# Optimization experiments

Hardware: AMD Instinct MI355X
Metric: run time of the kernel (lower is better)

## Reference

```python
import jax, jax.numpy as jnp
import numpy as np

HEAD_DIM = 64
NUM_HEADS = 32
ROPE_BASE = 10000.0


def _rope_interleaved(x):
    # x: [B, T, H, D]; interleaved RoPE on query, seqlen_offset = 0
    B, T, H, D = x.shape
    inv_freq = 1.0 / (ROPE_BASE ** (jnp.arange(0, D, 2, dtype=jnp.float32) / D))  # [D/2]
    t = jnp.arange(T, dtype=jnp.float32)
    freqs = t[:, None] * inv_freq[None, :]          # [T, D/2]
    cos = jnp.cos(freqs)[None, :, None, :]          # [1, T, 1, D/2]
    sin = jnp.sin(freqs)[None, :, None, :]
    x1 = x[..., 0::2]
    x2 = x[..., 1::2]
    o1 = x1 * cos - x2 * sin
    o2 = x1 * sin + x2 * cos
    out = jnp.stack([o1, o2], axis=-1).reshape(x.shape)  # re-interleave
    return out


def setup_inputs() -> dict:
    key = jax.random.key(0)
    k1, k2, k3, k4, k5 = jax.random.split(key, 5)
    B, T, Dm = 2, 2048, 2048
    H, Dh = NUM_HEADS, HEAD_DIM
    scale = 0.02
    return {
        "hidden_states": jax.random.normal(k1, (B, T, Dm), jnp.float32),
        "shared_k": jax.random.normal(k2, (B, T, H, Dh), jnp.float32),
        "shared_v": jax.random.normal(k3, (B, T, H, Dh), jnp.float32),
        "Wq": jax.random.normal(k4, (Dm, Dm), jnp.float32) * scale,
        "Wo": jax.random.normal(k5, (Dm, Dm), jnp.float32) * scale,
    }


def reference(hidden_states, shared_k, shared_v, Wq, Wo):
    B, T, Dm = hidden_states.shape
    H, Dh = NUM_HEADS, HEAD_DIM
    # q projection (nn.Linear: x @ W.T)
    q = (hidden_states @ Wq.T).reshape(B, T, H, Dh)
    # rotary on q only (seqlen_offset = shared_k_len - q_len = 0)
    q = _rope_interleaved(q)
    # parallel causal attention over shared KV cache (window_size=None)
    scale = 1.0 / jnp.sqrt(jnp.asarray(Dh, jnp.float32))
    scores = jnp.einsum('bqhd,bkhd->bhqk', q, shared_k) * scale
    causal = jnp.tril(jnp.ones((T, T), dtype=bool))
    scores = jnp.where(causal[None, None], scores, -jnp.inf)
    p = jax.nn.softmax(scores, axis=-1)
    o = jnp.einsum('bhqk,bkhd->bqhd', p, shared_v)
    o = o.reshape(B, T, Dm)
    return o @ Wo.T
```

## Files before the change

kernel.cpp:

```cpp
#include <hip/hip_runtime.h>
#include <stdint.h>

typedef short short8 __attribute__((ext_vector_type(8)));
typedef float f32x4 __attribute__((ext_vector_type(4)));

#define QSCALE 0.1803368801111137f

__device__ __forceinline__ float bf2f(unsigned short u) {
    union { unsigned int i; float f; } x; x.i = ((unsigned int)u) << 16; return x.f;
}
__device__ __forceinline__ unsigned short f2bf(float f) {
    union { float f; unsigned int i; } x; x.f = f;
    unsigned int i = x.i;
    unsigned int r = i + 0x7FFFu + ((i >> 16) & 1u);
    return (unsigned short)(r >> 16);
}

#define GLDS16(g, l) \
    __builtin_amdgcn_global_load_lds((const __attribute__((address_space(1))) void*)(g), \
                                     (__attribute__((address_space(3))) void*)(l), 16, 0, 0)

__global__ void cvt_f32_bf16(const float* __restrict__ in, unsigned short* __restrict__ out, int n4) {
    int i = blockIdx.x * 256 + threadIdx.x;
    if (i >= n4) return;
    float4 v = ((const float4*)in)[i];
    ushort4 o;
    o.x = f2bf(v.x); o.y = f2bf(v.y); o.z = f2bf(v.z); o.w = f2bf(v.w);
    ((ushort4*)out)[i] = o;
}

__global__ __launch_bounds__(256) void transpose_v(const float* __restrict__ V, unsigned short* __restrict__ Vt) {
    __shared__ float s[64 * 65];
    int t0 = blockIdx.x * 64;
    int bh = blockIdx.y;
    int b = bh >> 5, h = bh & 31;
    int tid = threadIdx.x;
#pragma unroll
    for (int it = 0; it < 4; ++it) {
        int c = tid + it * 256;
        int t = c >> 4;
        int d0 = (c & 15) * 4;
        float4 v = *(const float4*)(V + (size_t)(((b * 2048 + t0 + t) * 32 + h)) * 64 + d0);
        s[t * 65 + d0 + 0] = v.x; s[t * 65 + d0 + 1] = v.y;
        s[t * 65 + d0 + 2] = v.z; s[t * 65 + d0 + 3] = v.w;
    }
    __syncthreads();
#pragma unroll
    for (int it = 0; it < 2; ++it) {
        int c = tid + it * 256;
        int d = c >> 3;
        int tt = (c & 7) * 8;
        short8 pk;
#pragma unroll
        for (int j = 0; j < 8; ++j) pk[j] = (short)f2bf(s[(tt + j) * 65 + d]);
        *(short8*)(Vt + (size_t)(bh * 64 + d) * 2048 + t0 + tt) = pk;
    }
}

__global__ void rope_table(float* __restrict__ ct, float* __restrict__ st) {
    int i = blockIdx.x * 256 + threadIdx.x;
    int t = i >> 5, fi = i & 31;
    float inv = powf(10000.0f, -(2.0f * (float)fi) / 64.0f);
    float ang = (float)t * inv;
    ct[i] = cosf(ang);
    st[i] = sinf(ang);
}

__global__ void rope_apply(unsigned short* __restrict__ Q, const float* __restrict__ ct, const float* __restrict__ st) {
    int p = blockIdx.x * 256 + threadIdx.x;
    int row = p >> 10;
    int j = p & 1023;
    int t = row & 2047;
    int h = j >> 5, fi = j & 31;
    int col = h * 64 + fi * 2;
    unsigned int* addr = (unsigned int*)(Q + (size_t)row * 2048 + col);
    unsigned int v = *addr;
    float x1 = bf2f((unsigned short)(v & 0xffffu));
    float x2 = bf2f((unsigned short)(v >> 16));
    float c = ct[t * 32 + fi], s = st[t * 32 + fi];
    float o1 = (x1 * c - x2 * s) * QSCALE;
    float o2 = (x1 * s + x2 * c) * QSCALE;
    *addr = (unsigned int)f2bf(o1) | ((unsigned int)f2bf(o2) << 16);
}

template <bool BF16_OUT>
__global__ __launch_bounds__(256) void gemm_bt(
    const unsigned short* __restrict__ A,
    const unsigned short* __restrict__ B,
    void* __restrict__ Cout,
    int M, int N, int K)
{
    __shared__ __align__(16) unsigned short lA[128 * 32];
    __shared__ __align__(16) unsigned short lB[128 * 32];
    int tid = threadIdx.x;
    int lane = tid & 63;
    int wave = tid >> 6;
    int wm = (wave >> 1) * 64, wn = (wave & 1) * 64;
    int m16 = lane & 15, q = lane >> 4;
    int rowBase = blockIdx.x * 128, colBase = blockIdx.y * 128;

    f32x4 acc[4][4] = {};

    int sRow = wave * 16 + (lane >> 2);
    int sCol = (lane & 3) * 8;
    const unsigned short* gA0 = A + (size_t)(rowBase + sRow) * K + sCol;
    const unsigned short* gA1 = gA0 + (size_t)64 * K;
    const unsigned short* gB0 = B + (size_t)(colBase + sRow) * K + sCol;
    const unsigned short* gB1 = gB0 + (size_t)64 * K;
    unsigned short* lA0 = &lA[(wave * 16) * 32];
    unsigned short* lA1 = &lA[(64 + wave * 16) * 32];
    unsigned short* lB0 = &lB[(wave * 16) * 32];
    unsigned short* lB1 = &lB[(64 + wave * 16) * 32];

    for (int k0 = 0; k0 < K; k0 += 32) {
        __syncthreads();
        GLDS16(gA0 + k0, lA0);
        GLDS16(gA1 + k0, lA1);
        GLDS16(gB0 + k0, lB0);
        GLDS16(gB1 + k0, lB1);
        __syncthreads();
        short8 af[4], bfr[4];
#pragma unroll
        for (int i = 0; i < 4; ++i) {
            af[i]  = *(const short8*)&lA[(wm + i * 16 + m16) * 32 + q * 8];
            bfr[i] = *(const short8*)&lB[(wn + i * 16 + m16) * 32 + q * 8];
        }
#pragma unroll
        for (int i = 0; i < 4; ++i)
#pragma unroll
            for (int jn = 0; jn < 4; ++jn)
                acc[i][jn] = __builtin_amdgcn_mfma_f32_16x16x32_bf16(af[i], bfr[jn], acc[i][jn], 0, 0, 0);
    }
#pragma unroll
    for (int i = 0; i < 4; ++i)
#pragma unroll
        for (int jn = 0; jn < 4; ++jn)
#pragma unroll
            for (int r = 0; r < 4; ++r) {
                int row = rowBase + wm + i * 16 + q * 4 + r;
                int col = colBase + wn + jn * 16 + m16;
                float v = acc[i][jn][r];
                if (BF16_OUT) ((unsigned short*)Cout)[(size_t)row * N + col] = f2bf(v);
                else          ((float*)Cout)[(size_t)row * N + col] = v;
            }
}

__global__ __launch_bounds__(256) void attn(
    const unsigned short* __restrict__ Q,
    const unsigned short* __restrict__ Kb,
    const unsigned short* __restrict__ Vt,
    unsigned short* __restrict__ O)
{
    const int SL = 80;
    __shared__ __align__(16) unsigned short sK[64 * SL];
    __shared__ __align__(16) unsigned short sV[64 * SL];
    __shared__ __align__(16) unsigned short sP[4][16 * SL];
    int tid = threadIdx.x, lane = tid & 63, w = tid >> 6;
    int m16 = lane & 15, q = lane >> 4;
    int flat = blockIdx.x;
    int qt = 31 - (flat >> 6);
    int bh = flat & 63;
    int b = bh >> 5, h = bh & 31;
    int qBase = qt * 64;

    size_t rowQ = (size_t)(b * 2048 + qBase + w * 16 + m16) * 2048 + h * 64 + q * 8;
    short8 aq0 = *(const short8*)(Q + rowQ);
    short8 aq1 = *(const short8*)(Q + rowQ + 32);

    float lrun[4] = {0.f, 0.f, 0.f, 0.f};
    f32x4 accO[4];
#pragma unroll
    for (int nt = 0; nt < 4; ++nt) { f32x4 z = {0.f, 0.f, 0.f, 0.f}; accO[nt] = z; }

    int cK = tid >> 3;
    int c8 = tid & 7;
    const unsigned short* kbase = Kb + (size_t)(b * 2048) * 2048 + h * 64;
    const unsigned short* vbase = Vt + (size_t)((b * 32 + h) * 64) * 2048;

    for (int kt = 0; kt <= qt; ++kt) {
        int kBase = kt * 64;
        __syncthreads();
#pragma unroll
        for (int it = 0; it < 2; ++it) {
            int row = cK + it * 32;
            *(float4*)&sK[row * SL + c8 * 8] =
                *(const float4*)(kbase + (size_t)(kBase + row) * 2048 + c8 * 8);
            *(float4*)&sV[row * SL + c8 * 8] =
                *(const float4*)(vbase + (size_t)row * 2048 + kBase + c8 * 8);
        }
        __syncthreads();

        f32x4 accS[4];
#pragma unroll
        for (int nt = 0; nt < 4; ++nt) {
            f32x4 z = {0.f, 0.f, 0.f, 0.f};
            short8 bk0 = *(const short8*)&sK[(nt * 16 + m16) * SL + q * 8];
            short8 bk1 = *(const short8*)&sK[(nt * 16 + m16) * SL + 32 + q * 8];
            z = __builtin_amdgcn_mfma_f32_16x16x32_bf16(aq0, bk0, z, 0, 0, 0);
            z = __builtin_amdgcn_mfma_f32_16x16x32_bf16(aq1, bk1, z, 0, 0, 0);
            accS[nt] = z;
        }

        bool diag = (kt == qt);
#pragma unroll
        for (int nt = 0; nt < 4; ++nt)
#pragma unroll
            for (int r = 0; r < 4; ++r) {
                float s = accS[nt][r];
                if (diag) {
                    int key = nt * 16 + m16;
                    int qi = w * 16 + q * 4 + r;
                    if (key > qi) s = -__builtin_inff();
                }
                float p = __builtin_amdgcn_exp2f(s);
                lrun[r] += p;
                sP[w][(q * 4 + r) * SL + nt * 16 + m16] = f2bf(p);
            }

        short8 ap0 = *(const short8*)&sP[w][m16 * SL + q * 8];
        short8 ap1 = *(const short8*)&sP[w][m16 * SL + 32 + q * 8];
#pragma unroll
        for (int nt = 0; nt < 4; ++nt) {
            short8 bv0 = *(const short8*)&sV[(nt * 16 + m16) * SL + q * 8];
            short8 bv1 = *(const short8*)&sV[(nt * 16 + m16) * SL + 32 + q * 8];
            accO[nt] = __builtin_amdgcn_mfma_f32_16x16x32_bf16(ap0, bv0, accO[nt], 0, 0, 0);
            accO[nt] = __builtin_amdgcn_mfma_f32_16x16x32_bf16(ap1, bv1, accO[nt], 0, 0, 0);
        }
    }

#pragma unroll
    for (int r = 0; r < 4; ++r) {
        float l = lrun[r];
        l += __shfl_xor(l, 1);
        l += __shfl_xor(l, 2);
        l += __shfl_xor(l, 4);
        l += __shfl_xor(l, 8);
        lrun[r] = 1.0f / l;
    }
#pragma unroll
    for (int nt = 0; nt < 4; ++nt)
#pragma unroll
        for (int r = 0; r < 4; ++r) {
            float v = accO[nt][r] * lrun[r];
            O[(size_t)(b * 2048 + qBase + w * 16 + q * 4 + r) * 2048 + h * 64 + nt * 16 + m16] = f2bf(v);
        }
}

extern "C" void kernel_launch(void* const* d_in, const int* in_sizes, int n_in,
                              void* d_out, int out_size, void* d_ws, size_t ws_size,
                              hipStream_t stream) {
    const float* hs = (const float*)d_in[0];
    const float* sk = (const float*)d_in[1];
    const float* sv = (const float*)d_in[2];
    const float* wq = (const float*)d_in[3];
    const float* wo = (const float*)d_in[4];
    float* out = (float*)d_out;

    char* ws = (char*)d_ws;
    unsigned short* hid_b = (unsigned short*)(ws);
    unsigned short* wq_b  = (unsigned short*)(ws + ((size_t)16 << 20));
    unsigned short* wo_b  = (unsigned short*)(ws + ((size_t)24 << 20));
    unsigned short* k_b   = (unsigned short*)(ws + ((size_t)32 << 20));
    unsigned short* vt_b  = (unsigned short*)(ws + ((size_t)48 << 20));
    unsigned short* q_b   = (unsigned short*)(ws + ((size_t)64 << 20));
    unsigned short* o_b   = (unsigned short*)(ws + ((size_t)80 << 20));
    float* ct = (float*)(ws + ((size_t)96 << 20));
    float* st = (float*)(ws + ((size_t)96 << 20) + (1 << 18));

    cvt_f32_bf16<<<8192, 256, 0, stream>>>(hs, hid_b, 2097152);
    cvt_f32_bf16<<<4096, 256, 0, stream>>>(wq, wq_b, 1048576);
    cvt_f32_bf16<<<4096, 256, 0, stream>>>(wo, wo_b, 1048576);
    cvt_f32_bf16<<<8192, 256, 0, stream>>>(sk, k_b, 2097152);
    transpose_v<<<dim3(32, 64), 256, 0, stream>>>(sv, vt_b);
    rope_table<<<256, 256, 0, stream>>>(ct, st);
    gemm_bt<true><<<dim3(32, 16), 256, 0, stream>>>(hid_b, wq_b, (void*)q_b, 4096, 2048, 2048);
    rope_apply<<<16384, 256, 0, stream>>>(q_b, ct, st);
    attn<<<2048, 256, 0, stream>>>(q_b, k_b, vt_b, o_b);
    gemm_bt<false><<<dim3(32, 16), 256, 0, stream>>>(o_b, wo_b, (void*)out, 4096, 2048, 2048);
}
```

Measured before the change: 355.8 us.

## Fuse conversions and RoPE into attention, pair causal q-tiles, widen GEMM K-tile

The four fp32-to-bf16 conversion launches become one kernel. The RoPE table and apply kernels are removed; rotary is now computed inline with fast sin/cos when Q fragments are loaded in attention. Each attention block handles a short and a long query tile (qt and 31-qt), sharing K/V tile loads between them and balancing causal work across 1024 blocks. The GEMM uses a 64-wide K step with XOR-swizzled LDS to cut barriers and bank conflicts. Fast __sinf/__cosf at positions up to 2047 may lose accuracy, and the extra accumulators add register pressure under launch_bounds(256,4).

```diff
diff --git a/kernel.cpp b/kernel.cpp
--- a/kernel.cpp
+++ b/kernel.cpp
@@ -5,6 +5,7 @@
 typedef float f32x4 __attribute__((ext_vector_type(4)));
 
 #define QSCALE 0.1803368801111137f
+#define FREQC 0.4152410118609203f
 
 __device__ __forceinline__ float bf2f(unsigned short u) {
     union { unsigned int i; float f; } x; x.i = ((unsigned int)u) << 16; return x.f;
@@ -20,9 +21,16 @@
     __builtin_amdgcn_global_load_lds((const __attribute__((address_space(1))) void*)(g), \
                                      (__attribute__((address_space(3))) void*)(l), 16, 0, 0)
 
-__global__ void cvt_f32_bf16(const float* __restrict__ in, unsigned short* __restrict__ out, int n4) {
-    int i = blockIdx.x * 256 + threadIdx.x;
-    if (i >= n4) return;
+__global__ void cvt_all(const float* __restrict__ hs, const float* __restrict__ k,
+                        const float* __restrict__ wq, const float* __restrict__ wo,
+                        unsigned short* __restrict__ hs_b, unsigned short* __restrict__ k_b,
+                        unsigned short* __restrict__ wq_b, unsigned short* __restrict__ wo_b) {
+    int blk = blockIdx.x;
+    const float* in; unsigned short* out; int i;
+    if (blk < 8192)        { in = hs; out = hs_b; i = blk * 256 + threadIdx.x; }
+    else if (blk < 16384)  { in = k;  out = k_b;  i = (blk - 8192) * 256 + threadIdx.x; }
+    else if (blk < 20480)  { in = wq; out = wq_b; i = (blk - 16384) * 256 + threadIdx.x; }
+    else                   { in = wo; out = wo_b; i = (blk - 20480) * 256 + threadIdx.x; }
     float4 v = ((const float4*)in)[i];
     ushort4 o;
     o.x = f2bf(v.x); o.y = f2bf(v.y); o.z = f2bf(v.z); o.w = f2bf(v.w);
@@ -57,32 +65,6 @@
     }
 }
 
-__global__ void rope_table(float* __restrict__ ct, float* __restrict__ st) {
-    int i = blockIdx.x * 256 + threadIdx.x;
-    int t = i >> 5, fi = i & 31;
-    float inv = powf(10000.0f, -(2.0f * (float)fi) / 64.0f);
-    float ang = (float)t * inv;
-    ct[i] = cosf(ang);
-    st[i] = sinf(ang);
-}
-
-__global__ void rope_apply(unsigned short* __restrict__ Q, const float* __restrict__ ct, const float* __restrict__ st) {
-    int p = blockIdx.x * 256 + threadIdx.x;
-    int row = p >> 10;
-    int j = p & 1023;
-    int t = row & 2047;
-    int h = j >> 5, fi = j & 31;
-    int col = h * 64 + fi * 2;
-    unsigned int* addr = (unsigned int*)(Q + (size_t)row * 2048 + col);
-    unsigned int v = *addr;
-    float x1 = bf2f((unsigned short)(v & 0xffffu));
-    float x2 = bf2f((unsigned short)(v >> 16));
-    float c = ct[t * 32 + fi], s = st[t * 32 + fi];
-    float o1 = (x1 * c - x2 * s) * QSCALE;
-    float o2 = (x1 * s + x2 * c) * QSCALE;
-    *addr = (unsigned int)f2bf(o1) | ((unsigned int)f2bf(o2) << 16);
-}
-
 template <bool BF16_OUT>
 __global__ __launch_bounds__(256) void gemm_bt(
     const unsigned short* __restrict__ A,
@@ -90,46 +72,45 @@
     void* __restrict__ Cout,
     int M, int N, int K)
 {
-    __shared__ __align__(16) unsigned short lA[128 * 32];
-    __shared__ __align__(16) unsigned short lB[128 * 32];
-    int tid = threadIdx.x;
-    int lane = tid & 63;
-    int wave = tid >> 6;
+    __shared__ __align__(16) unsigned short lA[128 * 64];
+    __shared__ __align__(16) unsigned short lB[128 * 64];
+    int tid = threadIdx.x, lane = tid & 63, wave = tid >> 6;
     int wm = (wave >> 1) * 64, wn = (wave & 1) * 64;
     int m16 = lane & 15, q = lane >> 4;
     int rowBase = blockIdx.x * 128, colBase = blockIdx.y * 128;
-
     f32x4 acc[4][4] = {};
 
-    int sRow = wave * 16 + (lane >> 2);
-    int sCol = (lane & 3) * 8;
-    const unsigned short* gA0 = A + (size_t)(rowBase + sRow) * K + sCol;
-    const unsigned short* gA1 = gA0 + (size_t)64 * K;
-    const unsigned short* gB0 = B + (size_t)(colBase + sRow) * K + sCol;
-    const unsigned short* gB1 = gB0 + (size_t)64 * K;
-    unsigned short* lA0 = &lA[(wave * 16) * 32];
-    unsigned short* lA1 = &lA[(64 + wave * 16) * 32];
-    unsigned short* lB0 = &lB[(wave * 16) * 32];
-    unsigned short* lB1 = &lB[(64 + wave * 16) * 32];
-
-    for (int k0 = 0; k0 < K; k0 += 32) {
-        __syncthreads();
-        GLDS16(gA0 + k0, lA0);
-        GLDS16(gA1 + k0, lA1);
-        GLDS16(gB0 + k0, lB0);
-        GLDS16(gB1 + k0, lB1);
-        __syncthreads();
-        short8 af[4], bfr[4];
+    int sr = lane >> 3;
+    int g  = (lane & 7) ^ sr;
+    const unsigned short* gAp = A + (size_t)(rowBase + wave * 32 + sr) * K + g * 8;
+    const unsigned short* gBp = B + (size_t)(colBase + wave * 32 + sr) * K + g * 8;
+    unsigned short* lAd = &lA[(wave * 32) * 64];
+    unsigned short* lBd = &lB[(wave * 32) * 64];
+
+    for (int k0 = 0; k0 < K; k0 += 64) {
+        __syncthreads();
 #pragma unroll
         for (int i = 0; i < 4; ++i) {
-            af[i]  = *(const short8*)&lA[(wm + i * 16 + m16) * 32 + q * 8];
-            bfr[i] = *(const short8*)&lB[(wn + i * 16 + m16) * 32 + q * 8];
-        }
-#pragma unroll
-        for (int i = 0; i < 4; ++i)
-#pragma unroll
-            for (int jn = 0; jn < 4; ++jn)
-                acc[i][jn] = __builtin_amdgcn_mfma_f32_16x16x32_bf16(af[i], bfr[jn], acc[i][jn], 0, 0, 0);
+            GLDS16(gAp + (size_t)(8 * i) * K + k0, lAd + (8 * i) * 64);
+            GLDS16(gBp + (size_t)(8 * i) * K + k0, lBd + (8 * i) * 64);
+        }
+        __syncthreads();
+#pragma unroll
+        for (int kk = 0; kk < 2; ++kk) {
+            short8 af[4], bfr[4];
+#pragma unroll
+            for (int i = 0; i < 4; ++i) {
+                int RA = wm + i * 16 + m16;
+                af[i]  = *(const short8*)&lA[RA * 64 + (((kk * 4 + q) ^ (RA & 7)) * 8)];
+                int RB = wn + i * 16 + m16;
+                bfr[i] = *(const short8*)&lB[RB * 64 + (((kk * 4 + q) ^ (RB & 7)) * 8)];
+            }
+#pragma unroll
+            for (int i = 0; i < 4; ++i)
+#pragma unroll
+                for (int jn = 0; jn < 4; ++jn)
+                    acc[i][jn] = __builtin_amdgcn_mfma_f32_16x16x32_bf16(af[i], bfr[jn], acc[i][jn], 0, 0, 0);
+        }
     }
 #pragma unroll
     for (int i = 0; i < 4; ++i)
@@ -145,51 +126,69 @@
             }
 }
 
-__global__ __launch_bounds__(256) void attn(
+__global__ __launch_bounds__(256, 4) void attn(
     const unsigned short* __restrict__ Q,
     const unsigned short* __restrict__ Kb,
     const unsigned short* __restrict__ Vt,
     unsigned short* __restrict__ O)
 {
-    const int SL = 80;
+    const int SL = 72;
     __shared__ __align__(16) unsigned short sK[64 * SL];
     __shared__ __align__(16) unsigned short sV[64 * SL];
     __shared__ __align__(16) unsigned short sP[4][16 * SL];
     int tid = threadIdx.x, lane = tid & 63, w = tid >> 6;
     int m16 = lane & 15, q = lane >> 4;
     int flat = blockIdx.x;
-    int qt = 31 - (flat >> 6);
-    int bh = flat & 63;
+    int bh = flat & 63, p = flat >> 6;
     int b = bh >> 5, h = bh & 31;
-    int qBase = qt * 64;
-
-    size_t rowQ = (size_t)(b * 2048 + qBase + w * 16 + m16) * 2048 + h * 64 + q * 8;
-    short8 aq0 = *(const short8*)(Q + rowQ);
-    short8 aq1 = *(const short8*)(Q + rowQ + 32);
-
-    float lrun[4] = {0.f, 0.f, 0.f, 0.f};
-    f32x4 accO[4];
-#pragma unroll
-    for (int nt = 0; nt < 4; ++nt) { f32x4 z = {0.f, 0.f, 0.f, 0.f}; accO[nt] = z; }
-
-    int cK = tid >> 3;
-    int c8 = tid & 7;
+    int qtA = 31 - p, qtB = p;
+
+    short8 aqA0, aqA1, aqB0, aqB1;
+    {
+        int tA = qtA * 64 + w * 16 + m16;
+        int tB = qtB * 64 + w * 16 + m16;
+        const unsigned short* rowA = Q + (size_t)(b * 2048 + tA) * 2048 + h * 64 + q * 8;
+        const unsigned short* rowB = Q + (size_t)(b * 2048 + tB) * 2048 + h * 64 + q * 8;
+        short8 a0 = *(const short8*)rowA, a1 = *(const short8*)(rowA + 32);
+        short8 b0 = *(const short8*)rowB, b1 = *(const short8*)(rowB + 32);
+        float tfA = (float)tA, tfB = (float)tB;
+#pragma unroll
+        for (int j = 0; j < 4; ++j) {
+            float inv0 = __builtin_amdgcn_exp2f(-FREQC * (float)(q * 4 + j));
+            float inv1 = __builtin_amdgcn_exp2f(-FREQC * (float)(16 + q * 4 + j));
+            float cA0 = __cosf(tfA * inv0), sA0 = __sinf(tfA * inv0);
+            float cA1 = __cosf(tfA * inv1), sA1 = __sinf(tfA * inv1);
+            float cB0 = __cosf(tfB * inv0), sB0 = __sinf(tfB * inv0);
+            float cB1 = __cosf(tfB * inv1), sB1 = __sinf(tfB * inv1);
+            float x1, x2;
+            x1 = bf2f((unsigned short)a0[2 * j]); x2 = bf2f((unsigned short)a0[2 * j + 1]);
+            aqA0[2 * j]     = (short)f2bf((x1 * cA0 - x2 * sA0) * QSCALE);
+            aqA0[2 * j + 1] = (short)f2bf((x1 * sA0 + x2 * cA0) * QSCALE);
+            x1 = bf2f((unsigned short)a1[2 * j]); x2 = bf2f((unsigned short)a1[2 * j + 1]);
+            aqA1[2 * j]     = (short)f2bf((x1 * cA1 - x2 * sA1) * QSCALE);
+            aqA1[2 * j + 1] = (short)f2bf((x1 * sA1 + x2 * cA1) * QSCALE);
+            x1 = bf2f((unsigned short)b0[2 * j]); x2 = bf2f((unsigned short)b0[2 * j + 1]);
+            aqB0[2 * j]     = (short)f2bf((x1 * cB0 - x2 * sB0) * QSCALE);
+            aqB0[2 * j + 1] = (short)f2bf((x1 * sB0 + x2 * cB0) * QSCALE);
+            x1 = bf2f((unsigned short)b1[2 * j]); x2 = bf2f((unsigned short)b1[2 * j + 1]);
+            aqB1[2 * j]     = (short)f2bf((x1 * cB1 - x2 * sB1) * QSCALE);
+            aqB1[2 * j + 1] = (short)f2bf((x1 * sB1 + x2 * cB1) * QSCALE);
+        }
+    }
+
+    float lrunA[4] = {0.f, 0.f, 0.f, 0.f}, lrunB[4] = {0.f, 0.f, 0.f, 0.f};
+    f32x4 accOA[4], accOB[4];
+#pragma unroll
+    for (int nt = 0; nt < 4; ++nt) {
+        f32x4 z = {0.f, 0.f, 0.f, 0.f};
+        accOA[nt] = z; accOB[nt] = z;
+    }
+
+    int cK = tid >> 3, c8 = tid & 7;
     const unsigned short* kbase = Kb + (size_t)(b * 2048) * 2048 + h * 64;
     const unsigned short* vbase = Vt + (size_t)((b * 32 + h) * 64) * 2048;
 
-    for (int kt = 0; kt <= qt; ++kt) {
-        int kBase = kt * 64;
-        __syncthreads();
-#pragma unroll
-        for (int it = 0; it < 2; ++it) {
-            int row = cK + it * 32;
-            *(float4*)&sK[row * SL + c8 * 8] =
-                *(const float4*)(kbase + (size_t)(kBase + row) * 2048 + c8 * 8);
-            *(float4*)&sV[row * SL + c8 * 8] =
-                *(const float4*)(vbase + (size_t)row * 2048 + kBase + c8 * 8);
-        }
-        __syncthreads();
-
+    auto process = [&](short8 aq0, short8 aq1, float* lrun, f32x4* accO, int qt, int kt) {
         f32x4 accS[4];
 #pragma unroll
         for (int nt = 0; nt < 4; ++nt) {
@@ -200,7 +199,6 @@
             z = __builtin_amdgcn_mfma_f32_16x16x32_bf16(aq1, bk1, z, 0, 0, 0);
             accS[nt] = z;
         }
-
         bool diag = (kt == qt);
 #pragma unroll
         for (int nt = 0; nt < 4; ++nt)
@@ -212,11 +210,10 @@
                     int qi = w * 16 + q * 4 + r;
                     if (key > qi) s = -__builtin_inff();
                 }
-                float p = __builtin_amdgcn_exp2f(s);
-                lrun[r] += p;
-                sP[w][(q * 4 + r) * SL + nt * 16 + m16] = f2bf(p);
+                float pv = __builtin_amdgcn_exp2f(s);
+                lrun[r] += pv;
+                sP[w][(q * 4 + r) * SL + nt * 16 + m16] = f2bf(pv);
             }
-
         short8 ap0 = *(const short8*)&sP[w][m16 * SL + q * 8];
         short8 ap1 = *(const short8*)&sP[w][m16 * SL + 32 + q * 8];
 #pragma unroll
@@ -226,23 +223,43 @@
             accO[nt] = __builtin_amdgcn_mfma_f32_16x16x32_bf16(ap0, bv0, accO[nt], 0, 0, 0);
             accO[nt] = __builtin_amdgcn_mfma_f32_16x16x32_bf16(ap1, bv1, accO[nt], 0, 0, 0);
         }
+    };
+
+    for (int kt = 0; kt <= qtA; ++kt) {
+        int kBase = kt * 64;
+        __syncthreads();
+#pragma unroll
+        for (int it = 0; it < 2; ++it) {
+            int row = cK + it * 32;
+            *(float4*)&sK[row * SL + c8 * 8] =
+                *(const float4*)(kbase + (size_t)(kBase + row) * 2048 + c8 * 8);
+            *(float4*)&sV[row * SL + c8 * 8] =
+                *(const float4*)(vbase + (size_t)row * 2048 + kBase + c8 * 8);
+        }
+        __syncthreads();
+
+        process(aqA0, aqA1, lrunA, accOA, qtA, kt);
+        if (kt <= qtB) process(aqB0, aqB1, lrunB, accOB, qtB, kt);
     }
 
 #pragma unroll
     for (int r = 0; r < 4; ++r) {
-        float l = lrun[r];
-        l += __shfl_xor(l, 1);
-        l += __shfl_xor(l, 2);
-        l += __shfl_xor(l, 4);
-        l += __shfl_xor(l, 8);
-        lrun[r] = 1.0f / l;
+        float la = lrunA[r], lb = lrunB[r];
+        la += __shfl_xor(la, 1); lb += __shfl_xor(lb, 1);
+        la += __shfl_xor(la, 2); lb += __shfl_xor(lb, 2);
+        la += __shfl_xor(la, 4); lb += __shfl_xor(lb, 4);
+        la += __shfl_xor(la, 8); lb += __shfl_xor(lb, 8);
+        lrunA[r] = 1.0f / la; lrunB[r] = 1.0f / lb;
     }
 #pragma unroll
     for (int nt = 0; nt < 4; ++nt)
 #pragma unroll
         for (int r = 0; r < 4; ++r) {
-            float v = accO[nt][r] * lrun[r];
-            O[(size_t)(b * 2048 + qBase + w * 16 + q * 4 + r) * 2048 + h * 64 + nt * 16 + m16] = f2bf(v);
+            int col = h * 64 + nt * 16 + m16;
+            O[(size_t)(b * 2048 + qtA * 64 + w * 16 + q * 4 + r) * 2048 + col] =
+                f2bf(accOA[nt][r] * lrunA[r]);
+            O[(size_t)(b * 2048 + qtB * 64 + w * 16 + q * 4 + r) * 2048 + col] =
+                f2bf(accOB[nt][r] * lrunB[r]);
         }
 }
 
@@ -264,17 +281,10 @@
     unsigned short* vt_b  = (unsigned short*)(ws + ((size_t)48 << 20));
     unsigned short* q_b   = (unsigned short*)(ws + ((size_t)64 << 20));
     unsigned short* o_b   = (unsigned short*)(ws + ((size_t)80 << 20));
-    float* ct = (float*)(ws + ((size_t)96 << 20));
-    float* st = (float*)(ws + ((size_t)96 << 20) + (1 << 18));
-
-    cvt_f32_bf16<<<8192, 256, 0, stream>>>(hs, hid_b, 2097152);
-    cvt_f32_bf16<<<4096, 256, 0, stream>>>(wq, wq_b, 1048576);
-    cvt_f32_bf16<<<4096, 256, 0, stream>>>(wo, wo_b, 1048576);
-    cvt_f32_bf16<<<8192, 256, 0, stream>>>(sk, k_b, 2097152);
+
+    cvt_all<<<24576, 256, 0, stream>>>(hs, sk, wq, wo, hid_b, k_b, wq_b, wo_b);
     transpose_v<<<dim3(32, 64), 256, 0, stream>>>(sv, vt_b);
-    rope_table<<<256, 256, 0, stream>>>(ct, st);
     gemm_bt<true><<<dim3(32, 16), 256, 0, stream>>>(hid_b, wq_b, (void*)q_b, 4096, 2048, 2048);
-    rope_apply<<<16384, 256, 0, stream>>>(q_b, ct, st);
-    attn<<<2048, 256, 0, stream>>>(q_b, k_b, vt_b, o_b);
+    attn<<<1024, 256, 0, stream>>>(q_b, k_b, vt_b, o_b);
     gemm_bt<false><<<dim3(32, 16), 256, 0, stream>>>(o_b, wo_b, (void*)out, 4096, 2048, 2048);
 }
```

After: 408.4 us. 14.8% more time.
